# Optimization experiments

Measured on AMD Instinct MI355X. Metric: run time of the kernel, lower is better.

The kernel has to match this reference:

```python
import jax, jax.numpy as jnp
import numpy as np
from jax import lax

B, CIN, HID, COUT = 64, 256, 256, 10
MULTI, KS = 3, 3
TH = TW = 7      # template (kernel) input spatial size
SH = SW = 31     # search input spatial size
EPS = 1e-5
DN = ('NCHW', 'OIHW', 'NCHW')


def _conv(x, w):
    return lax.conv_general_dilated(x, w, (1, 1), 'VALID', dimension_numbers=DN)


def _bn(x, p):
    # p: [4, C] packed (gamma, beta, running_mean, running_var); inference-mode BN
    g, b, m, v = p[0], p[1], p[2], p[3]
    inv = g / jnp.sqrt(v + EPS)
    return x * inv[:, None, None] + (b - m * inv)[:, None, None]


def _dwxcorr(x, k):
    # per-sample depthwise cross-correlation via groups = B*C trick
    b, c, h, w = x.shape
    kh, kw = k.shape[2], k.shape[3]
    y = lax.conv_general_dilated(
        x.reshape(1, b * c, h, w), k.reshape(b * c, 1, kh, kw),
        (1, 1), 'VALID', dimension_numbers=DN, feature_group_count=b * c)
    return y.reshape(b, c, y.shape[2], y.shape[3])


def _multixcorr(search, kernel):
    # crop template feature to 5x5 / 3x3 / 1x1 sub-kernels, xcorr each,
    # center-crop outputs to the common (smallest) size, concat on channels
    kh = kernel.shape[2]
    feats = []
    for i in range(MULTI):
        kk = kernel[:, :, i:kh - i, i:kh - i]
        o = _dwxcorr(search, kk)
        if i > 0:
            o = o[:, :, i:o.shape[2] - i, i:o.shape[3] - i]
        feats.append(o)
    return jnp.concatenate(feats, axis=1)  # [B, MULTI*HID, 25, 25]


def setup_inputs() -> dict:
    key = jax.random.key(0)
    ks = jax.random.split(key, 12)
    f32 = jnp.float32
    return {
        'kernel': jax.random.normal(ks[0], (B, CIN, TH, TW), f32),
        'search': jax.random.normal(ks[1], (B, CIN, SH, SW), f32),
        'wk': jax.random.normal(ks[2], (HID, CIN, KS, KS), f32) * 0.05,
        'bnk': jax.random.uniform(ks[3], (4, HID), f32, 0.1, 1.0),
        'ws': jax.random.normal(ks[4], (HID, CIN, KS, KS), f32) * 0.05,
        'bns': jax.random.uniform(ks[5], (4, HID), f32, 0.1, 1.0),
        'wd': jax.random.normal(ks[6], (HID, CIN * MULTI, 1, 1), f32) * 0.05,
        'bnd': jax.random.uniform(ks[7], (4, HID), f32, 0.1, 1.0),
        'wh1': jax.random.normal(ks[8], (HID, HID, 1, 1), f32) * 0.05,
        'bnh': jax.random.uniform(ks[9], (4, HID), f32, 0.1, 1.0),
        'wh2': jax.random.normal(ks[10], (COUT, HID, 1, 1), f32) * 0.05,
        'bh2': jax.random.normal(ks[11], (COUT,), f32) * 0.05,
    }


def reference(kernel, search, wk, bnk, ws, bns, wd, bnd, wh1, bnh, wh2, bh2):
    k = jax.nn.relu(_bn(_conv(kernel, wk), bnk))   # [B, HID, 5, 5]
    s = jax.nn.relu(_bn(_conv(search, ws), bns))   # [B, HID, 29, 29]
    feature = _multixcorr(s, k)                    # [B, 3*HID, 25, 25]
    feature = _bn(_conv(feature, wd), bnd)         # [B, HID, 25, 25]
    h = jax.nn.relu(_bn(_conv(feature, wh1), bnh))
    out = _conv(h, wh2) + bh2[:, None, None]       # [B, COUT, 25, 25]
    return out
```

## Files before the change

kernel.cpp:

```cpp
#include <hip/hip_runtime.h>
#include <hip/hip_bf16.h>
#include <cstdint>
#include <cstddef>

#define EPSBN 1e-5f

typedef unsigned short u16;
typedef unsigned int u32;
typedef _Float16 f16;
typedef _Float16 f16x8 __attribute__((ext_vector_type(8)));
typedef float f32x4 __attribute__((ext_vector_type(4)));

__device__ __forceinline__ void async_copy16(void* lds, const void* g) {
    __builtin_amdgcn_global_load_lds(
        (const __attribute__((address_space(1))) u32*)g,
        (__attribute__((address_space(3))) u32*)lds, 16, 0, 0);
}

__global__ __launch_bounds__(256) void prep_all(
    const float* __restrict__ sin, f16* __restrict__ sa,
    const float* __restrict__ kin, f16* __restrict__ ka,
    const float* __restrict__ wk, const float* __restrict__ ws,
    const float* __restrict__ wd, const float* __restrict__ wh1,
    const float* __restrict__ wh2, f16* __restrict__ bpk,
    f16* __restrict__ bps, f16* __restrict__ bpd, f16* __restrict__ bp1,
    f16* __restrict__ bp2) {
    __shared__ float tile[64][65];
    int t = blockIdx.x;
    int tid = threadIdx.x;
    if (t < 4352) {
        int b = t / 68;
        int rem = t - b * 68;
        int c0 = (rem / 17) * 64;
        int z = rem % 17;
        bool isk = (z == 16);
        const float* in = isk ? kin : sin;
        f16* op = isk ? ka : sa;
        int HW = isk ? 49 : 961;
        int h0 = isk ? 0 : z * 64;
        int cl = tid >> 6;
        int hl = tid & 63;
        for (int r = cl; r < 64; r += 4) {
            int hw = h0 + hl;
            tile[r][hl] =
                (hw < HW) ? in[(size_t)(b * 256 + c0 + r) * HW + hw] : 0.f;
        }
        __syncthreads();
        int c = tid & 63;
        for (int r = cl; r < 64; r += 4) {
            int hw = h0 + r;
            if (hw < HW)
                op[((size_t)b * HW + hw) * 256 + c0 + c] = (f16)tile[c][r];
        }
        return;
    }
    int blk = t - 4352;
    const float* W;
    f16* Bp;
    int nK32, OCr, K, i;
    bool conv = false;
    if (blk < 2304) {
        W = wk; Bp = bpk; nK32 = 72; OCr = 256; K = 2304; conv = true;
        i = blk * 256 + tid;
    } else if (blk < 4608) {
        W = ws; Bp = bps; nK32 = 72; OCr = 256; K = 2304; conv = true;
        i = (blk - 2304) * 256 + tid;
    } else if (blk < 5376) {
        W = wd; Bp = bpd; nK32 = 24; OCr = 256; K = 768;
        i = (blk - 4608) * 256 + tid;
    } else if (blk < 5632) {
        W = wh1; Bp = bp1; nK32 = 8; OCr = 256; K = 256;
        i = (blk - 5376) * 256 + tid;
    } else {
        W = wh2; Bp = bp2; nK32 = 8; OCr = 10; K = 256;
        i = (blk - 5632) * 256 + tid;
    }
    int per = nK32 * 512;
    int oct = i / per;
    int r = i - oct * per;
    int k32 = r >> 9;
    int lr = r & 511;
    int l = lr >> 3, j = lr & 7;
    int oc = oct * 16 + (l & 15);
    int k = k32 * 32 + ((l >> 4) << 3) + j;
    float v = 0.f;
    if (oc < OCr)
        v = conv ? W[(size_t)(oc * 256 + (k & 255)) * 9 + (k >> 8)]
                 : W[(size_t)oc * K + k];
    Bp[(size_t)(oct * nK32 + k32) * 512 + lr] = (f16)v;
}

template <int KHW, int EPI>
__device__ __forceinline__ void gemm_body(
    f16* sA, const f16* __restrict__ A, const f16* __restrict__ Bp,
    const float* __restrict__ bnp, float* __restrict__ outF,
    f16* __restrict__ oF, int m0, int n0, int M, int OC, int C, int H, int W,
    int OH, int OW) {
    const int Ktot = KHW * C;
    const int nKb = Ktot >> 7;
    const int nK32 = Ktot >> 5;
    const int tid = threadIdx.x;
    const int OHW = OH * OW;

    int abase[8];
#pragma unroll
    for (int s = 0; s < 8; ++s) {
        int idx = tid + s * 256;
        int ml = idx >> 4;
        int qs = (idx & 15) ^ (ml & 15);
        int m = m0 + ml;
        if (m >= M) m = M - 1;
        int b = m / OHW;
        int r = m - b * OHW;
        int y = r / OW;
        int x = r - y * OW;
        abase[s] = ((b * H + y) * W + x) * C + qs * 8;
    }

    f32x4 acc[4][4];
#pragma unroll
    for (int i = 0; i < 4; ++i)
#pragma unroll
        for (int j = 0; j < 4; ++j) acc[i][j] = (f32x4)0.f;

    const int lane = tid & 63;
    const int row = lane & 15;
    const int quad = lane >> 4;
    const int wv = tid >> 6;
    const int wm = (wv & 1) * 64;
    const int wn = (wv >> 1) * 64;
    const int octb = (n0 + wn) >> 4;

    auto koff_of = [&](int kb) {
        if (KHW == 9) {
            int pos = kb >> 1;
            int cin0 = (kb & 1) << 7;
            int ky = pos / 3;
            int kx = pos - ky * 3;
            return (ky * W + kx) * C + cin0;
        }
        return kb << 7;
    };
    auto issueA = [&](int bufbase, int kb) {
        int koff = koff_of(kb);
#pragma unroll
        for (int s = 0; s < 8; ++s)
            async_copy16(&sA[bufbase + tid * 8 + s * 2048],
                         A + abase[s] + koff);
    };
    auto loadB = [&](f16x8(&bh)[4][4], int kb) {
#pragma unroll
        for (int ks = 0; ks < 4; ++ks)
#pragma unroll
            for (int j = 0; j < 4; ++j)
                bh[ks][j] =
                    *(const f16x8*)&Bp[((size_t)(octb + j) * nK32 + kb * 4 +
                                        ks) *
                                           512 +
                                       lane * 8];
    };
    auto compute = [&](int bufbase, f16x8(&bh)[4][4]) {
#pragma unroll
        for (int ks = 0; ks < 4; ++ks) {
            f16x8 ah[4];
#pragma unroll
            for (int i = 0; i < 4; ++i) {
                int g = wm + i * 16 + row;
                ah[i] = *(const f16x8*)&sA[bufbase + g * 128 +
                                           ((((ks << 2) | quad) ^ row) << 3)];
            }
#pragma unroll
            for (int i = 0; i < 4; ++i)
#pragma unroll
                for (int j = 0; j < 4; ++j)
                    acc[i][j] = __builtin_amdgcn_mfma_f32_16x16x32_f16(
                        ah[i], bh[ks][j], acc[i][j], 0, 0, 0);
        }
    };

    f16x8 bh0[4][4], bh1[4][4];
    issueA(0, 0);
    loadB(bh0, 0);
    for (int kb = 0; kb < nKb; kb += 2) {
        __syncthreads();
        issueA(16384, kb + 1);
        loadB(bh1, kb + 1);
        compute(0, bh0);
        __syncthreads();
        if (kb + 2 < nKb) {
            issueA(0, kb + 2);
            loadB(bh0, kb + 2);
        }
        compute(16384, bh1);
    }

#pragma unroll
    for (int j = 0; j < 4; ++j) {
        int oc = n0 + wn + j * 16 + row;
        bool ocv = oc < OC;
        float scale = 1.f, shift = 0.f;
        if (ocv) {
            if (EPI != 3) {
                float g = bnp[oc];
                float bb = bnp[OC + oc];
                float mm = bnp[2 * OC + oc];
                float vv = bnp[3 * OC + oc];
                float inv = g * rsqrtf(vv + EPSBN);
                scale = inv;
                shift = bb - mm * inv;
            } else {
                shift = bnp[oc];
            }
        }
#pragma unroll
        for (int i = 0; i < 4; ++i) {
#pragma unroll
            for (int r = 0; r < 4; ++r) {
                int m = m0 + wm + i * 16 + quad * 4 + r;
                if (m < M && ocv) {
                    float v = acc[i][j][r] * scale + shift;
                    if (EPI == 2) v = fmaxf(v, 0.f);
                    if (EPI == 3) {
                        int b = m / OHW;
                        int rr = m - b * OHW;
                        outF[((size_t)b * OC + oc) * OHW + rr] = v;
                    } else {
                        oF[(size_t)m * OC + oc] = (f16)v;
                    }
                }
            }
        }
    }
}

__global__ __launch_bounds__(256, 2) void conv33_fused(
    const f16* sA_g, const f16* bpS, const float* bns, f16* sOut,
    const f16* kA_g, const f16* bpK, const float* bnk, f16* kOut) {
    __shared__ f16 sA[32768];
    bool sec = blockIdx.x < 13;
    const f16* A = sec ? kA_g : sA_g;
    const f16* Bp = sec ? bpK : bpS;
    const float* bnp = sec ? bnk : bns;
    f16* oF = sec ? kOut : sOut;
    int M = sec ? 1600 : 53824;
    int H = sec ? 7 : 31;
    int OHs = sec ? 5 : 29;
    int m0 = (sec ? blockIdx.x : (blockIdx.x - 13)) * 128;
    int n0 = blockIdx.y * 128;
    gemm_body<9, 2>(sA, A, Bp, bnp, nullptr, oF, m0, n0, M, 256, 256, H, H,
                    OHs, OHs);
}

template <int EPI>
__global__ __launch_bounds__(256, 2) void gemm_1x1(
    const f16* __restrict__ A, const f16* __restrict__ Bp,
    const float* __restrict__ bnp, float* __restrict__ outF,
    f16* __restrict__ oF, int M, int OC, int C) {
    __shared__ f16 sA[32768];
    gemm_body<1, EPI>(sA, A, Bp, bnp, outF, oF, blockIdx.x * 128,
                      blockIdx.y * 128, M, OC, C, 25, 25, 25, 25);
}

__global__ __launch_bounds__(256) void xcorr_nhwc(
    const f16* __restrict__ sf, const f16* __restrict__ kf,
    f16* __restrict__ feat) {
    int by = blockIdx.x;
    int b = by / 25;
    int y = by - b * 25;
    int c = threadIdx.x;
    float kv[25];
#pragma unroll
    for (int p = 0; p < 25; ++p)
        kv[p] = (float)kf[(size_t)(b * 25 + p) * 256 + c];
    const f16* srow = sf + (size_t)(b * 29 + y) * 29 * 256 + c;
    float sv[25];
#pragma unroll
    for (int d = 0; d < 5; ++d)
#pragma unroll
        for (int e = 0; e < 5; ++e)
            sv[d * 5 + e] = (float)srow[(size_t)(d * 29 + e) * 256];
    for (int x = 0;; ++x) {
        float a0 = 0.f, a1 = 0.f, a2;
#pragma unroll
        for (int p = 0; p < 25; ++p) a0 = fmaf(sv[p], kv[p], a0);
#pragma unroll
        for (int d = 1; d < 4; ++d)
#pragma unroll
            for (int e = 1; e < 4; ++e)
                a1 = fmaf(sv[d * 5 + e], kv[d * 5 + e], a1);
        a2 = sv[12] * kv[12];
        size_t o = ((size_t)by * 25 + x) * 768 + c;
        feat[o] = (f16)a0;
        feat[o + 256] = (f16)a1;
        feat[o + 512] = (f16)a2;
        if (x == 24) break;
#pragma unroll
        for (int d = 0; d < 5; ++d) {
#pragma unroll
            for (int e = 0; e < 4; ++e) sv[d * 5 + e] = sv[d * 5 + e + 1];
            sv[d * 5 + 4] = (float)srow[(size_t)(d * 29 + x + 5) * 256];
        }
    }
}

extern "C" void kernel_launch(void* const* d_in, const int* in_sizes, int n_in,
                              void* d_out, int out_size, void* d_ws,
                              size_t ws_size, hipStream_t stream) {
    const float* kernel_in = (const float*)d_in[0];
    const float* search_in = (const float*)d_in[1];
    const float* wk = (const float*)d_in[2];
    const float* bnk = (const float*)d_in[3];
    const float* ws = (const float*)d_in[4];
    const float* bns = (const float*)d_in[5];
    const float* wd = (const float*)d_in[6];
    const float* bnd = (const float*)d_in[7];
    const float* wh1 = (const float*)d_in[8];
    const float* bnh = (const float*)d_in[9];
    const float* wh2 = (const float*)d_in[10];
    const float* bh2 = (const float*)d_in[11];
    float* out = (float*)d_out;

    char* base = (char*)d_ws;
    size_t off = 0;
    auto alloc = [&](size_t bytes) {
        off = (off + 511) & ~(size_t)511;
        void* p = base + off;
        off += bytes;
        return p;
    };

    f16* bpd = (f16*)alloc((size_t)16 * 24 * 512 * 2);
    f16* bp1 = (f16*)alloc((size_t)16 * 8 * 512 * 2);
    f16* bp2 = (f16*)alloc((size_t)8 * 8 * 512 * 2);
    size_t Pf = (off + 511) & ~(size_t)511;
    f16* kfeat = (f16*)alloc((size_t)1600 * 256 * 2);
    f16* sfeat = (f16*)alloc((size_t)53824 * 256 * 2);
    size_t P1 = (off + 511) & ~(size_t)511;
    f16* bpk = (f16*)alloc((size_t)16 * 72 * 512 * 2);
    f16* bps = (f16*)alloc((size_t)16 * 72 * 512 * 2);
    f16* ka = (f16*)alloc((size_t)64 * 49 * 256 * 2);
    f16* sa = (f16*)alloc((size_t)64 * 961 * 256 * 2);
    f16* feat = (f16*)(base + P1);
    f16* f2 = (f16*)(base + Pf);
    f16* hb = (f16*)(base + P1);

    prep_all<<<dim3(10112), 256, 0, stream>>>(search_in, sa, kernel_in, ka,
                                              wk, ws, wd, wh1, wh2, bpk, bps,
                                              bpd, bp1, bp2);
    conv33_fused<<<dim3(434, 2), 256, 0, stream>>>(sa, bps, bns, sfeat, ka,
                                                   bpk, bnk, kfeat);
    xcorr_nhwc<<<dim3(1600), 256, 0, stream>>>(sfeat, kfeat, feat);
    gemm_1x1<1><<<dim3(313, 2), 256, 0, stream>>>(feat, bpd, bnd, nullptr, f2,
                                                  40000, 256, 768);
    gemm_1x1<2><<<dim3(313, 2), 256, 0, stream>>>(f2, bp1, bnh, nullptr, hb,
                                                  40000, 256, 256);
    gemm_1x1<3><<<dim3(313, 1), 256, 0, stream>>>(hb, bp2, bh2, out, nullptr,
                                                  40000, 10, 256);
}
```

Measured before the change: 329.1 us.

## Replace 3x3 conv GEMM with 256x256-tile 8-wave double-buffered pipelined kernel

Swaps the 128x128-tile, 4-wave implicit-GEMM for the two 3x3 convolutions for a new 8-wave kernel. Each block computes a 256x256 tile covering all output channels, and the grid drops from 434x2 to 218 blocks. The new kernel double-buffers A and B in 128 KB of LDS with async global-to-LDS copies interleaved between MFMA quadrants, using setprio and explicit waitcnt/barriers to overlap loads with compute. This aims to improve data reuse and hide memory latency in the dominant conv stage, at the cost of heavy register pressure (128 accumulators per lane), large LDS use per block, and fewer blocks for load balancing.

```diff
diff --git a/kernel.cpp b/kernel.cpp
--- a/kernel.cpp
+++ b/kernel.cpp
@@ -91,6 +91,234 @@
 }
 
 template <int KHW, int EPI>
+__device__ __forceinline__ void gemm8_body(
+    f16* lds, const f16* __restrict__ A, const f16* __restrict__ Bp,
+    const float* __restrict__ bnp, float* __restrict__ outF,
+    f16* __restrict__ oF, int m0, int M, int OC, int C, int H, int W,
+    int OH, int OW) {
+    const int Ktot = KHW * C;
+    const int nKt = Ktot >> 6;
+    const int nI = nKt >> 1;
+    const int nK32 = Ktot >> 5;
+    const int tid = threadIdx.x;
+    const int lane = tid & 63;
+    const int wid = tid >> 6;
+    const int rowl = lane & 15;
+    const int quad = lane >> 4;
+    const int wm = wid >> 2;
+    const int wn = wid & 3;
+    const int OHW = OH * OW;
+
+    int arow[4];
+#pragma unroll
+    for (int h = 0; h < 2; ++h)
+#pragma unroll
+        for (int s = 0; s < 2; ++s) {
+            int ml = ((wid & 4) << 5) + h * 64 + (wid & 3) * 16 + s * 8 +
+                     (lane >> 3);
+            int m = m0 + ml;
+            if (m >= M) m = M - 1;
+            int b = m / OHW;
+            int r = m - b * OHW;
+            int y = r / OW;
+            int x = r - y * OW;
+            arow[h * 2 + s] = ((b * H + y) * W + x) * C +
+                              (((lane & 7) ^ (lane >> 3)) << 3);
+        }
+    int bsrcb[2];
+#pragma unroll
+    for (int h = 0; h < 2; ++h) {
+        int slot = h * 8 + wid;
+        int o = ((slot >> 1) & 3) * 4 + ((slot >> 3) << 1) + (slot & 1);
+        bsrcb[h] = o * nK32 * 512 + lane * 8;
+    }
+
+    auto koff_of = [&](int kt) {
+        if (KHW == 9) {
+            int pos = kt >> 2;
+            int ky = pos / 3, kx = pos - ky * 3;
+            return (ky * W + kx) * C + ((kt & 3) << 6);
+        }
+        return kt << 6;
+    };
+    auto stageA = [&](int buf, int h, int kt) {
+        int koff = koff_of(kt);
+#pragma unroll
+        for (int s = 0; s < 2; ++s)
+            async_copy16(
+                &lds[buf * 16384 +
+                     ((h * 1024 + wid * 128 + s * 64 + lane) << 3)],
+                A + arow[h * 2 + s] + koff);
+    };
+    auto stageB = [&](int buf, int h, int kt) {
+#pragma unroll
+        for (int s = 0; s < 2; ++s)
+            async_copy16(
+                &lds[32768 + buf * 16384 +
+                     ((((h * 8 + wid) * 2 + s) * 64 + lane) << 3)],
+                Bp + bsrcb[h] + (kt * 2 + s) * 512);
+    };
+
+    f32x4 acc[8][4];
+#pragma unroll
+    for (int i = 0; i < 8; ++i)
+#pragma unroll
+        for (int j = 0; j < 4; ++j) acc[i][j] = (f32x4)0.f;
+
+    f16x8 ah[4][2], bhA[2][2], bhB[2][2];
+
+    auto dsA = [&](int buf, int qm) {
+#pragma unroll
+        for (int ii = 0; ii < 4; ++ii) {
+            int g = qm * 128 + wm * 64 + ii * 16 + rowl;
+#pragma unroll
+            for (int ks = 0; ks < 2; ++ks)
+                ah[ii][ks] = *(const f16x8*)&lds[
+                    buf * 16384 + g * 64 +
+                    ((((ks << 2) | quad) ^ (rowl & 7)) << 3)];
+        }
+    };
+    auto dsB = [&](int buf, int qn, f16x8 (&bh)[2][2]) {
+#pragma unroll
+        for (int jj = 0; jj < 2; ++jj) {
+            int slot = qn * 8 + wn * 2 + jj;
+#pragma unroll
+            for (int ks = 0; ks < 2; ++ks)
+                bh[jj][ks] = *(const f16x8*)&lds[
+                    32768 + buf * 16384 + (slot * 2 + ks) * 512 + lane * 8];
+        }
+    };
+
+#define MFMA_QUAD(qm, qn, bh)                                            \
+    do {                                                                 \
+        _Pragma("unroll") for (int ks = 0; ks < 2; ++ks)                 \
+            _Pragma("unroll") for (int ii = 0; ii < 4; ++ii)             \
+                _Pragma("unroll") for (int jj = 0; jj < 2; ++jj)         \
+                    acc[(qm)*4 + ii][(qn)*2 + jj] =                      \
+                        __builtin_amdgcn_mfma_f32_16x16x32_f16(          \
+                            ah[ii][ks], bh[jj][ks],                      \
+                            acc[(qm)*4 + ii][(qn)*2 + jj], 0, 0, 0);     \
+    } while (0)
+
+#define PH_TAIL(MF)                                        \
+    __builtin_amdgcn_s_barrier();                          \
+    asm volatile("s_waitcnt lgkmcnt(0)" ::: "memory");     \
+    __builtin_amdgcn_s_setprio(1);                         \
+    MF;                                                    \
+    __builtin_amdgcn_s_setprio(0)
+
+    stageA(0, 0, 0);
+    stageA(0, 1, 0);
+    stageB(0, 0, 0);
+    stageB(0, 1, 0);
+    stageA(1, 0, 1);
+    stageB(1, 0, 1);
+    stageB(1, 1, 1);
+    asm volatile("s_waitcnt vmcnt(6)" ::: "memory");
+    __builtin_amdgcn_s_barrier();
+
+    for (int it = 0; it < nI; ++it) {
+        const bool more = (it + 1 < nI);
+        const int t2 = 2 * it + 2;
+        const int t3 = 2 * it + 3;
+        dsA(0, 0);
+        dsB(0, 0, bhA);
+        stageA(1, 1, 2 * it + 1);
+        PH_TAIL(MFMA_QUAD(0, 0, bhA));
+        __builtin_amdgcn_s_barrier();
+        dsB(0, 1, bhB);
+        if (more) stageA(0, 0, t2);
+        PH_TAIL(MFMA_QUAD(0, 1, bhB));
+        __builtin_amdgcn_s_barrier();
+        dsA(0, 1);
+        if (more) stageB(0, 0, t2);
+        PH_TAIL(MFMA_QUAD(1, 0, bhA));
+        __builtin_amdgcn_s_barrier();
+        if (more) stageB(0, 1, t2);
+        PH_TAIL(MFMA_QUAD(1, 1, bhB));
+        if (more)
+            asm volatile("s_waitcnt vmcnt(6)" ::: "memory");
+        else
+            asm volatile("s_waitcnt vmcnt(0)" ::: "memory");
+        __builtin_amdgcn_s_barrier();
+        dsA(1, 0);
+        dsB(1, 0, bhA);
+        if (more) stageA(0, 1, t2);
+        PH_TAIL(MFMA_QUAD(0, 0, bhA));
+        __builtin_amdgcn_s_barrier();
+        dsB(1, 1, bhB);
+        if (more) stageA(1, 0, t3);
+        PH_TAIL(MFMA_QUAD(0, 1, bhB));
+        __builtin_amdgcn_s_barrier();
+        dsA(1, 1);
+        if (more) stageB(1, 0, t3);
+        PH_TAIL(MFMA_QUAD(1, 0, bhA));
+        __builtin_amdgcn_s_barrier();
+        if (more) stageB(1, 1, t3);
+        PH_TAIL(MFMA_QUAD(1, 1, bhB));
+        if (more) asm volatile("s_waitcnt vmcnt(6)" ::: "memory");
+        __builtin_amdgcn_s_barrier();
+    }
+#undef PH_TAIL
+#undef MFMA_QUAD
+
+#pragma unroll
+    for (int j = 0; j < 4; ++j) {
+        int oc = wn * 64 + j * 16 + rowl;
+        bool ocv = oc < OC;
+        float scale = 1.f, shift = 0.f;
+        if (ocv) {
+            if (EPI != 3) {
+                float g = bnp[oc];
+                float bb = bnp[OC + oc];
+                float mm = bnp[2 * OC + oc];
+                float vv = bnp[3 * OC + oc];
+                float inv = g * rsqrtf(vv + EPSBN);
+                scale = inv;
+                shift = bb - mm * inv;
+            } else {
+                shift = bnp[oc];
+            }
+        }
+#pragma unroll
+        for (int i = 0; i < 8; ++i) {
+#pragma unroll
+            for (int r = 0; r < 4; ++r) {
+                int m = m0 + wm * 128 + i * 16 + quad * 4 + r;
+                if (m < M && ocv) {
+                    float v = acc[i][j][r] * scale + shift;
+                    if (EPI == 2) v = fmaxf(v, 0.f);
+                    if (EPI == 3) {
+                        int b = m / OHW;
+                        int rr = m - b * OHW;
+                        outF[((size_t)b * OC + oc) * OHW + rr] = v;
+                    } else {
+                        oF[(size_t)m * OC + oc] = (f16)v;
+                    }
+                }
+            }
+        }
+    }
+}
+
+__global__ __launch_bounds__(512, 2) void conv33_fused8(
+    const f16* sA_g, const f16* bpS, const float* bns, f16* sOut,
+    const f16* kA_g, const f16* bpK, const float* bnk, f16* kOut) {
+    __shared__ f16 lds[65536];
+    bool sec = blockIdx.x < 7;
+    const f16* A = sec ? kA_g : sA_g;
+    const f16* Bp = sec ? bpK : bpS;
+    const float* bnp = sec ? bnk : bns;
+    f16* oF = sec ? kOut : sOut;
+    int M = sec ? 1600 : 53824;
+    int Hh = sec ? 7 : 31;
+    int OHs = sec ? 5 : 29;
+    int m0 = (sec ? blockIdx.x : (blockIdx.x - 7)) * 256;
+    gemm8_body<9, 2>(lds, A, Bp, bnp, nullptr, oF, m0, M, 256, 256, Hh, Hh,
+                     OHs, OHs);
+}
+
+template <int KHW, int EPI>
 __device__ __forceinline__ void gemm_body(
     f16* sA, const f16* __restrict__ A, const f16* __restrict__ Bp,
     const float* __restrict__ bnp, float* __restrict__ outF,
@@ -233,24 +461,6 @@
     }
 }
 
-__global__ __launch_bounds__(256, 2) void conv33_fused(
-    const f16* sA_g, const f16* bpS, const float* bns, f16* sOut,
-    const f16* kA_g, const f16* bpK, const float* bnk, f16* kOut) {
-    __shared__ f16 sA[32768];
-    bool sec = blockIdx.x < 13;
-    const f16* A = sec ? kA_g : sA_g;
-    const f16* Bp = sec ? bpK : bpS;
-    const float* bnp = sec ? bnk : bns;
-    f16* oF = sec ? kOut : sOut;
-    int M = sec ? 1600 : 53824;
-    int H = sec ? 7 : 31;
-    int OHs = sec ? 5 : 29;
-    int m0 = (sec ? blockIdx.x : (blockIdx.x - 13)) * 128;
-    int n0 = blockIdx.y * 128;
-    gemm_body<9, 2>(sA, A, Bp, bnp, nullptr, oF, m0, n0, M, 256, 256, H, H,
-                    OHs, OHs);
-}
-
 template <int EPI>
 __global__ __launch_bounds__(256, 2) void gemm_1x1(
     const f16* __restrict__ A, const f16* __restrict__ Bp,
@@ -347,8 +557,8 @@
     prep_all<<<dim3(10112), 256, 0, stream>>>(search_in, sa, kernel_in, ka,
                                               wk, ws, wd, wh1, wh2, bpk, bps,
                                               bpd, bp1, bp2);
-    conv33_fused<<<dim3(434, 2), 256, 0, stream>>>(sa, bps, bns, sfeat, ka,
-                                                   bpk, bnk, kfeat);
+    conv33_fused8<<<dim3(218), 512, 0, stream>>>(sa, bps, bns, sfeat, ka,
+                                                 bpk, bnk, kfeat);
     xcorr_nhwc<<<dim3(1600), 256, 0, stream>>>(sfeat, kfeat, feat);
     gemm_1x1<1><<<dim3(313, 2), 256, 0, stream>>>(feat, bpd, bnd, nullptr, f2,
                                                   40000, 256, 768);
```

Result: faster. 312.1 us (-5.2%).
